# Optimization experiments

Measured on AMD Instinct MI355X. Metric: run time of the kernel, lower is better.

Reference implementation:

```python
import jax, jax.numpy as jnp
import numpy as np

B, G, K, A = 2, 50000, 32, 64  # batch, grid points, neighbors, ao_vals


def setup_inputs() -> dict:
    key = jax.random.key(0)
    k1, k2, k3, k4 = jax.random.split(key, 4)
    out = jax.random.normal(k1, (B, G, A), dtype=jnp.float32)
    # neighbor indices in [0, G]; index G points at the zero padding row
    coords_neighbors_idx = jax.random.randint(k2, (G, K), 0, G + 1, dtype=jnp.int32)
    scale = 1.0 / np.sqrt(A)
    W2 = jax.random.normal(k3, (A, A), dtype=jnp.float32) * scale
    b2 = jnp.zeros((A,), dtype=jnp.float32)
    W3 = jax.random.normal(k4, (A, A), dtype=jnp.float32) * scale
    b3 = jnp.zeros((A,), dtype=jnp.float32)
    return {"out": out, "coords_neighbors_idx": coords_neighbors_idx,
            "W2": W2, "b2": b2, "W3": W3, "b3": b3}


def reference(out, coords_neighbors_idx, W2, b2, W3, b3):
    n_batch, n_grid, n_ao = out.shape
    # pad grid axis with a zero row so index n_grid gathers zeros
    pad = jnp.concatenate([out, jnp.zeros((n_batch, 1, n_ao), out.dtype)], axis=1)
    # gather neighbors: [B, G, K, A], then sum-aggregate over neighbors
    messages = jnp.take(pad, coords_neighbors_idx, axis=1).sum(axis=2)  # [B, G, A]
    messages = messages @ W2 + b2  # dense_2 (activation=None)
    y = out + messages             # residual
    y = y @ W3 + b3                # dense_3 (activation=None)
    return y
```

## Files before the change

kernel.cpp:

```cpp
#include <hip/hip_runtime.h>
#include <hip/hip_fp16.h>


constexpr int A = 64;
constexpr int K = 32;

__global__ void w23_kernel(const float* __restrict__ W2, const float* __restrict__ b2,
                           const float* __restrict__ W3, const float* __restrict__ b3,
                           float* __restrict__ W23, float* __restrict__ bb) {
  const int e = blockIdx.x * 256 + threadIdx.x;
  const int i = e >> 6, j = e & 63;
  float acc = 0.f;
#pragma unroll
  for (int q = 0; q < A; ++q) acc = fmaf(W2[i * A + q], W3[q * A + j], acc);
  W23[e] = acc;
  if (blockIdx.x == 0 && threadIdx.x < A) {
    const int t = threadIdx.x;
    float b = b3[t];
#pragma unroll
    for (int q = 0; q < A; ++q) b = fmaf(b2[q], W3[q * A + t], b);
    bb[t] = b;
  }
}

__global__ void pack_kernel(const float2* __restrict__ out2,
                            __half2* __restrict__ packed, const int G) {
  const int d = blockIdx.x * 256 + threadIdx.x;
  const int total = (G + 1) * 64;
  if (d >= total) return;
  const int g = d >> 6, c = d & 63;
  float2 v = make_float2(0.f, 0.f);
  if (g < G) {
    const int b = c >> 5;
    v = out2[(size_t)b * (G * 32) + (size_t)g * 32 + (c & 31)];
  }
  packed[d] = __floats2half2_rn(v.x, v.y);
}

__device__ __forceinline__ float bcastf(float x, int l) {
  return __int_as_float(__builtin_amdgcn_readlane(__float_as_int(x), l));
}

__global__ __launch_bounds__(256, 5) void fused_kernel(
    const __half2* __restrict__ packed, const int* __restrict__ nbr,
    const float* __restrict__ W23, const float* __restrict__ W3,
    const float* __restrict__ bb, float* __restrict__ y, const int G) {
  __shared__ float WI[A * 128];
  const int tid = threadIdx.x;
  for (int e = tid; e < A * 128; e += 256) {
    const int i = e >> 7, c = e & 127;
    WI[e] = (c < A) ? W23[i * A + c] : W3[i * A + (c - A)];
  }
  __syncthreads();

  const int lane = tid & 63;
  const int g = __builtin_amdgcn_readfirstlane(blockIdx.x * 4 + (tid >> 6));
  if (g >= G) return;

  const int* np = nbr + g * K;

  float mx = 0.f, my = 0.f;
#pragma unroll
  for (int k = 0; k < K; ++k) {
    const int j = np[k];
    const float2 u = __half22float2(packed[(size_t)j * 64 + lane]);
    mx += u.x; my += u.y;
  }
  const float2 o = __half22float2(packed[(size_t)g * 64 + lane]);
  const float bbv = bb[lane];

  float ya0 = bbv, yb0 = 0.f, ya1 = bbv, yb1 = 0.f;
#pragma unroll
  for (int i = 0; i < A; ++i) {
    const int s0 = i >> 1, s1 = 32 + (i >> 1);
    const float w2c = WI[i * 128 + lane];
    const float w3c = WI[i * 128 + A + lane];
    const float m0v = bcastf((i & 1) ? my : mx, s0);
    const float m1v = bcastf((i & 1) ? my : mx, s1);
    const float o0v = bcastf((i & 1) ? o.y : o.x, s0);
    const float o1v = bcastf((i & 1) ? o.y : o.x, s1);
    ya0 = fmaf(m0v, w2c, ya0);
    ya1 = fmaf(m1v, w2c, ya1);
    yb0 = fmaf(o0v, w3c, yb0);
    yb1 = fmaf(o1v, w3c, yb1);
  }

  const int GA = G * A;
  y[g * A + lane]      = ya0 + yb0;
  y[GA + g * A + lane] = ya1 + yb1;
}

extern "C" void kernel_launch(void* const* d_in, const int* in_sizes, int n_in,
                              void* d_out, int out_size, void* d_ws, size_t ws_size,
                              hipStream_t stream) {
  const float* out = (const float*)d_in[0];
  const int*   nbr = (const int*)d_in[1];
  const float* W2  = (const float*)d_in[2];
  const float* b2  = (const float*)d_in[3];
  const float* W3  = (const float*)d_in[4];
  const float* b3  = (const float*)d_in[5];
  float* y = (float*)d_out;
  const int G = in_sizes[1] / K;

  __half2* packed = (__half2*)d_ws;
  const size_t packedBytes = (size_t)(G + 1) * 64 * sizeof(__half2);
  float* W23 = (float*)((char*)d_ws + packedBytes);
  float* bb  = W23 + A * A;

  w23_kernel<<<16, 256, 0, stream>>>(W2, b2, W3, b3, W23, bb);

  const int packTotal = (G + 1) * 64;
  pack_kernel<<<(packTotal + 255) / 256, 256, 0, stream>>>(
      (const float2*)out, packed, G);

  const int blocks = (G + 3) / 4;
  fused_kernel<<<blocks, 256, 0, stream>>>(packed, nbr, W23, W3, bb, y, G);
}
```

Measured before the change: 168.1 us.

## Replace per-grid-point FMA matmul with MFMA tiles over 32 grid points per block

Each block now gathers and sums neighbors for 32 grid points into an fp16 shared tile, then computes the fused [m|o]·[W23;W3] projection with 16x16x32 f16 MFMA instructions instead of readlane-broadcast scalar FMAs. Neighbor accumulation switches to half2 adds with four partial accumulators, and weights are pre-transposed to fp16. This removes the per-point weight-tile reload and the scalar FMA loop, at the cost of fp16 accumulation and fp16 weights lowering precision, plus lower occupancy from the larger shared memory footprint.

```diff
diff --git a/kernel.cpp b/kernel.cpp
--- a/kernel.cpp
+++ b/kernel.cpp
@@ -2,18 +2,24 @@
 #include <hip/hip_fp16.h>
 
 
-constexpr int A = 64;
-constexpr int K = 32;
+constexpr int A  = 64;
+constexpr int K  = 32;
+constexpr int GPB = 32;
+constexpr int XS = 136;
 
-__global__ void w23_kernel(const float* __restrict__ W2, const float* __restrict__ b2,
-                           const float* __restrict__ W3, const float* __restrict__ b3,
-                           float* __restrict__ W23, float* __restrict__ bb) {
+typedef _Float16 f16x8 __attribute__((ext_vector_type(8)));
+typedef float    f32x4 __attribute__((ext_vector_type(4)));
+
+__global__ void wprep_kernel(const float* __restrict__ W2, const float* __restrict__ b2,
+                             const float* __restrict__ W3, const float* __restrict__ b3,
+                             __half* __restrict__ WTg, float* __restrict__ bb) {
   const int e = blockIdx.x * 256 + threadIdx.x;
-  const int i = e >> 6, j = e & 63;
+  const int n = e >> 6, k = e & 63;
   float acc = 0.f;
 #pragma unroll
-  for (int q = 0; q < A; ++q) acc = fmaf(W2[i * A + q], W3[q * A + j], acc);
-  W23[e] = acc;
+  for (int q = 0; q < A; ++q) acc = fmaf(W2[k * A + q], W3[q * A + n], acc);
+  WTg[n * 128 + k]     = __float2half(acc);
+  WTg[n * 128 + A + k] = __float2half(W3[k * A + n]);
   if (blockIdx.x == 0 && threadIdx.x < A) {
     const int t = threadIdx.x;
     float b = b3[t];
@@ -37,57 +43,95 @@
   packed[d] = __floats2half2_rn(v.x, v.y);
 }
 
-__device__ __forceinline__ float bcastf(float x, int l) {
-  return __int_as_float(__builtin_amdgcn_readlane(__float_as_int(x), l));
-}
+__global__ __launch_bounds__(256, 4) void fused_kernel(
+    const __half2* __restrict__ packed, const int* __restrict__ nbr,
+    const __half* __restrict__ WTg, const float* __restrict__ bb,
+    float* __restrict__ y, const int G) {
+  __shared__ __half X[64 * XS];
+  __shared__ __half WT[64 * XS];
 
-__global__ __launch_bounds__(256, 5) void fused_kernel(
-    const __half2* __restrict__ packed, const int* __restrict__ nbr,
-    const float* __restrict__ W23, const float* __restrict__ W3,
-    const float* __restrict__ bb, float* __restrict__ y, const int G) {
-  __shared__ float WI[A * 128];
   const int tid = threadIdx.x;
-  for (int e = tid; e < A * 128; e += 256) {
-    const int i = e >> 7, c = e & 127;
-    WI[e] = (c < A) ? W23[i * A + c] : W3[i * A + (c - A)];
+
+  {
+    const unsigned int* src = (const unsigned int*)WTg;
+    unsigned int* dst = (unsigned int*)WT;
+#pragma unroll
+    for (int s = 0; s < 16; ++s) {
+      const int d = s * 256 + tid;
+      const int n = d >> 6, c = d & 63;
+      dst[n * (XS / 2) + c] = src[d];
+    }
+  }
+
+  const int lane = tid & 63;
+  const int w = __builtin_amdgcn_readfirstlane(tid >> 6);
+  const int gbase = blockIdx.x * GPB;
+  const int gcount = min(GPB, G - gbase);
+  const int e = lane & 31;
+  const int rb = (lane >> 5) * 32;
+
+  const __half2 z = __floats2half2_rn(0.f, 0.f);
+
+#pragma unroll
+  for (int gg = 0; gg < 8; ++gg) {
+    const int gl = w * 8 + gg;
+    if (gl < gcount) {
+      const int g = gbase + gl;
+      const int* np = nbr + g * K;
+      __half2 m0 = z, m1 = z, m2 = z, m3 = z;
+#pragma unroll
+      for (int k = 0; k < K; k += 4) {
+        const __half2 u0 = packed[(size_t)np[k]     * 64 + lane];
+        const __half2 u1 = packed[(size_t)np[k + 1] * 64 + lane];
+        const __half2 u2 = packed[(size_t)np[k + 2] * 64 + lane];
+        const __half2 u3 = packed[(size_t)np[k + 3] * 64 + lane];
+        m0 = __hadd2(m0, u0);
+        m1 = __hadd2(m1, u1);
+        m2 = __hadd2(m2, u2);
+        m3 = __hadd2(m3, u3);
+      }
+      const __half2 m = __hadd2(__hadd2(m0, m1), __hadd2(m2, m3));
+      const __half2 o = packed[(size_t)g * 64 + lane];
+      const int r = rb + gl;
+      *(__half2*)&X[r * XS + 2 * e]     = m;
+      *(__half2*)&X[r * XS + A + 2 * e] = o;
+    }
   }
   __syncthreads();
 
-  const int lane = tid & 63;
-  const int g = __builtin_amdgcn_readfirstlane(blockIdx.x * 4 + (tid >> 6));
-  if (g >= G) return;
-
-  const int* np = nbr + g * K;
-
-  float mx = 0.f, my = 0.f;
+  const int quad = lane >> 4;
+  const int mn = lane & 15;
+  f32x4 acc0 = {0.f, 0.f, 0.f, 0.f};
+  f32x4 acc1 = {0.f, 0.f, 0.f, 0.f};
+  f32x4 acc2 = {0.f, 0.f, 0.f, 0.f};
+  f32x4 acc3 = {0.f, 0.f, 0.f, 0.f};
 #pragma unroll
-  for (int k = 0; k < K; ++k) {
-    const int j = np[k];
-    const float2 u = __half22float2(packed[(size_t)j * 64 + lane]);
-    mx += u.x; my += u.y;
-  }
-  const float2 o = __half22float2(packed[(size_t)g * 64 + lane]);
-  const float bbv = bb[lane];
-
-  float ya0 = bbv, yb0 = 0.f, ya1 = bbv, yb1 = 0.f;
-#pragma unroll
-  for (int i = 0; i < A; ++i) {
-    const int s0 = i >> 1, s1 = 32 + (i >> 1);
-    const float w2c = WI[i * 128 + lane];
-    const float w3c = WI[i * 128 + A + lane];
-    const float m0v = bcastf((i & 1) ? my : mx, s0);
-    const float m1v = bcastf((i & 1) ? my : mx, s1);
-    const float o0v = bcastf((i & 1) ? o.y : o.x, s0);
-    const float o1v = bcastf((i & 1) ? o.y : o.x, s1);
-    ya0 = fmaf(m0v, w2c, ya0);
-    ya1 = fmaf(m1v, w2c, ya1);
-    yb0 = fmaf(o0v, w3c, yb0);
-    yb1 = fmaf(o1v, w3c, yb1);
+  for (int kt = 0; kt < 4; ++kt) {
+    const int ko = kt * 32 + quad * 8;
+    const f16x8 a = *(const f16x8*)&X[(w * 16 + mn) * XS + ko];
+    const f16x8 b0 = *(const f16x8*)&WT[(0 * 16 + mn) * XS + ko];
+    acc0 = __builtin_amdgcn_mfma_f32_16x16x32_f16(a, b0, acc0, 0, 0, 0);
+    const f16x8 b1 = *(const f16x8*)&WT[(1 * 16 + mn) * XS + ko];
+    acc1 = __builtin_amdgcn_mfma_f32_16x16x32_f16(a, b1, acc1, 0, 0, 0);
+    const f16x8 b2 = *(const f16x8*)&WT[(2 * 16 + mn) * XS + ko];
+    acc2 = __builtin_amdgcn_mfma_f32_16x16x32_f16(a, b2, acc2, 0, 0, 0);
+    const f16x8 b3 = *(const f16x8*)&WT[(3 * 16 + mn) * XS + ko];
+    acc3 = __builtin_amdgcn_mfma_f32_16x16x32_f16(a, b3, acc3, 0, 0, 0);
   }
 
-  const int GA = G * A;
-  y[g * A + lane]      = ya0 + yb0;
-  y[GA + g * A + lane] = ya1 + yb1;
+  f32x4 accs[4] = {acc0, acc1, acc2, acc3};
+#pragma unroll
+  for (int nt = 0; nt < 4; ++nt) {
+    const int col = nt * 16 + mn;
+    const float bv = bb[col];
+#pragma unroll
+    for (int rg = 0; rg < 4; ++rg) {
+      const int row = w * 16 + quad * 4 + rg;
+      const int b = row >> 5, gl = row & 31;
+      if (gl < gcount)
+        y[((size_t)b * G + (gbase + gl)) * 64 + col] = accs[nt][rg] + bv;
+    }
+  }
 }
 
 extern "C" void kernel_launch(void* const* d_in, const int* in_sizes, int n_in,
@@ -104,15 +148,15 @@
 
   __half2* packed = (__half2*)d_ws;
   const size_t packedBytes = (size_t)(G + 1) * 64 * sizeof(__half2);
-  float* W23 = (float*)((char*)d_ws + packedBytes);
-  float* bb  = W23 + A * A;
+  __half* WTg = (__half*)((char*)d_ws + packedBytes);
+  float* bb = (float*)((char*)d_ws + packedBytes + 8192 * sizeof(__half));
 
-  w23_kernel<<<16, 256, 0, stream>>>(W2, b2, W3, b3, W23, bb);
+  wprep_kernel<<<16, 256, 0, stream>>>(W2, b2, W3, b3, WTg, bb);
 
   const int packTotal = (G + 1) * 64;
   pack_kernel<<<(packTotal + 255) / 256, 256, 0, stream>>>(
       (const float2*)out, packed, G);
 
-  const int blocks = (G + 3) / 4;
-  fused_kernel<<<blocks, 256, 0, stream>>>(packed, nbr, W23, W3, bb, y, G);
+  const int blocks = (G + GPB - 1) / GPB;
+  fused_kernel<<<blocks, 256, 0, stream>>>(packed, nbr, WTg, bb, y, G);
 }
```

New measurement: 144.4 us. 1.16x faster.
